# Kernel tuning notes

Measured on AMD Instinct MI355X. Metric: run time of the kernel, lower is better.

## Reference

```python
import jax, jax.numpy as jnp
import numpy as np

B, IN, H = 4096, 1024, 2048


def setup_inputs() -> dict:
    key = jax.random.key(0)
    k1, k2, k3, k4 = jax.random.split(key, 4)
    x = jax.random.normal(k1, (B, IN), dtype=jnp.float32)
    h_prev = jax.random.normal(k2, (B, H), dtype=jnp.float32)
    c_prev = jax.random.normal(k3, (B, H), dtype=jnp.float32)
    # Fused weight for the 5 gate Linears (Wf, Wi, Wc, Wo, We), columns stacked.
    # Scaled like PyTorch Linear default init (~uniform(-1/sqrt(fan_in))).
    W = jax.random.normal(k4, (IN + H, 5 * H), dtype=jnp.float32) / jnp.sqrt(jnp.float32(IN + H))
    b = jnp.zeros((5 * H,), dtype=jnp.float32)
    return {"x": x, "h_prev": h_prev, "c_prev": c_prev, "W": W, "b": b}


def reference(x, h_prev, c_prev, W, b):
    combined = jnp.concatenate([x, h_prev], axis=1)          # [B, IN+H]
    z = combined @ W + b                                      # [B, 5H] single fused GEMM
    f, i, c_hat, o, e = jnp.split(z, 5, axis=1)
    ft = jax.nn.sigmoid(f)
    it = jax.nn.sigmoid(i)
    ct_hat = jnp.tanh(c_hat)
    ot = jax.nn.sigmoid(o)
    et = jax.nn.sigmoid(e)
    ct = ft * c_prev + it * ct_hat
    ht = ot * jnp.tanh(ct)
    ht = et * jnp.exp(ht) + (1.0 - et) * ht
    return ht, ct
```

## Files before the change

### kernel.cpp

```cpp
#include <hip/hip_runtime.h>
#include <hip/hip_bf16.h>
#include <stdint.h>

#define B_  4096
#define IN_ 1024
#define H_  2048
#define K_  (IN_ + H_)
#define N_  (5 * H_)

#define BM 128
#define BJ 32
#define BK 32
#define NT 96

typedef __attribute__((ext_vector_type(8))) short   short8;
typedef __attribute__((ext_vector_type(4))) float   f32x4;
typedef __attribute__((ext_vector_type(8))) unsigned short ushort8;

__device__ __forceinline__ unsigned short f2bf(float f) {
  union { float f; unsigned u; } cv; cv.f = f;
  unsigned u = cv.u;
  u += 0x7fffu + ((u >> 16) & 1u);
  return (unsigned short)(u >> 16);
}

__device__ __forceinline__ void async16(const unsigned short* g, unsigned short* l) {
  __builtin_amdgcn_global_load_lds(
      (const __attribute__((address_space(1))) unsigned int*)g,
      (__attribute__((address_space(3))) unsigned int*)(void*)l,
      16, 0, 0);
}

__device__ __forceinline__ float fsig(float x) {
  return __builtin_amdgcn_rcpf(1.f + __expf(-x));
}
__device__ __forceinline__ float ftanh(float x) {
  return 1.f - 2.f * __builtin_amdgcn_rcpf(__expf(2.f * x) + 1.f);
}

__global__ void build_combined(const float* __restrict__ x,
                               const float* __restrict__ h,
                               unsigned short* __restrict__ out) {
  const int row = blockIdx.x;
  const float4* xr = (const float4*)(x + (size_t)row * IN_);
  const float4* hr = (const float4*)(h + (size_t)row * H_);
  uint2* orow = (uint2*)(out + (size_t)row * K_);
  for (int c = threadIdx.x; c < K_ / 4; c += 256) {
    float4 v = (c < IN_ / 4) ? xr[c] : hr[c - IN_ / 4];
    uint2 p;
    p.x = (unsigned)f2bf(v.x) | ((unsigned)f2bf(v.y) << 16);
    p.y = (unsigned)f2bf(v.z) | ((unsigned)f2bf(v.w) << 16);
    orow[c] = p;
  }
}

__global__ __launch_bounds__(256) void transpose_convert(
    const float* __restrict__ W, unsigned short* __restrict__ Wt) {
  __shared__ float tile[64][65];
  const int n0 = blockIdx.x * 64;
  const int k0 = blockIdx.y * 64;
  const int t  = threadIdx.x;

  const int r0 = t >> 4;
  const int c4 = t & 15;
  #pragma unroll
  for (int i = 0; i < 4; ++i) {
    const int kk = i * 16 + r0;
    const float4 v = *(const float4*)&W[(size_t)(k0 + kk) * N_ + n0 + c4 * 4];
    float* dst = &tile[kk][c4 * 4];
    dst[0] = v.x; dst[1] = v.y; dst[2] = v.z; dst[3] = v.w;
  }
  __syncthreads();

  #pragma unroll
  for (int i = 0; i < 2; ++i) {
    const int c2 = t + i * 256;
    const int nn = c2 >> 3;
    const int kc = (c2 & 7) * 8;
    ushort8 p;
    #pragma unroll
    for (int u = 0; u < 8; ++u) p[u] = f2bf(tile[kc + u][nn]);
    *(ushort8*)&Wt[(size_t)(n0 + nn) * K_ + k0 + kc] = p;
  }
}

__global__ __launch_bounds__(256, 3) void gemm_fused(
    const unsigned short* __restrict__ A,
    const unsigned short* __restrict__ Bt,
    const float* __restrict__ c_prev,
    const float* __restrict__ bias,
    float* __restrict__ out)
{
  __shared__ unsigned short As[2][BM * BK];
  __shared__ unsigned short Bs[2][5 * BJ * BK];

  const int tid  = threadIdx.x;
  const int wave = tid >> 6;
  const int lane = tid & 63;
  const int quad = lane >> 4;
  const int lr   = lane & 15;

  const int tile_m = blockIdx.x >> 6;
  const int tile_j = blockIdx.x & 63;
  const int m0 = tile_m * BM;
  const int j0 = tile_j * BJ;

  const int wm = (wave & 1) * 64;
  const int wn = (wave >> 1) * 16;

  f32x4 acc[4][5];
  #pragma unroll
  for (int mi = 0; mi < 4; ++mi)
    #pragma unroll
    for (int g = 0; g < 5; ++g)
      acc[mi][g] = (f32x4){0.f, 0.f, 0.f, 0.f};

  const int lrow4 = lane >> 2;
  const int scol  = ((lane & 3) ^ ((lane >> 3) & 3)) * 8;
  const size_t k16 = (size_t)16 * K_;

  const unsigned short* aP =
      A + ((size_t)(m0 + wave * 32 + lrow4)) * K_ + scol;
  const int aL0o = (wave * 32) * BK;
  const int aL1o = (wave * 32 + 16) * BK;

  const unsigned short* bBase = Bt + ((size_t)(j0 + lrow4)) * K_ + scol;
  const unsigned short* bP0 = bBase + (size_t)wave * H_ * K_;
  const unsigned short* bP2 = bBase + ((size_t)4 * H_ + wave * 16) * K_;
  const int bL0o = (wave * 32) * BK;
  const int bL1o = (wave * 32 + 16) * BK;
  const int bL2o = ((8 + wave) * 16) * BK;
  const bool doTail = (wave < 2);

  #define STAGE(tt, bb) do {                          \
    const int ko_ = (tt) * BK;                        \
    async16(aP + ko_,        &As[(bb)][aL0o]);        \
    async16(aP + k16 + ko_,  &As[(bb)][aL1o]);        \
    async16(bP0 + ko_,       &Bs[(bb)][bL0o]);        \
    async16(bP0 + k16 + ko_, &Bs[(bb)][bL1o]);        \
    if (doTail) async16(bP2 + ko_, &Bs[(bb)][bL2o]);  \
  } while (0)

  STAGE(0, 0);
  STAGE(1, 1);

  const int rslot = (quad ^ ((lr >> 1) & 3)) * 8;

  #pragma unroll 2
  for (int t = 0; t < NT; ++t) {
    const int cur = t & 1;

    if (t == NT - 1)     asm volatile("s_waitcnt vmcnt(0)" ::: "memory");
    else if (doTail)     asm volatile("s_waitcnt vmcnt(5)" ::: "memory");
    else                 asm volatile("s_waitcnt vmcnt(4)" ::: "memory");
    __builtin_amdgcn_s_barrier();

    short8 af[4], bf[5];
    #pragma unroll
    for (int mi = 0; mi < 4; ++mi)
      af[mi] = *(const short8*)&As[cur][(wm + mi * 16 + lr) * BK + rslot];
    #pragma unroll
    for (int g = 0; g < 5; ++g)
      bf[g] = *(const short8*)&Bs[cur][(g * 32 + wn + lr) * BK + rslot];

    asm volatile("s_waitcnt lgkmcnt(0)" ::: "memory");
    __builtin_amdgcn_sched_barrier(0);
    __builtin_amdgcn_s_barrier();

    if (t < NT - 2) STAGE(t + 2, cur);
    __builtin_amdgcn_sched_barrier(0);

    __builtin_amdgcn_s_setprio(1);
    #pragma unroll
    for (int mi = 0; mi < 4; ++mi)
      #pragma unroll
      for (int g = 0; g < 5; ++g)
        acc[mi][g] = __builtin_amdgcn_mfma_f32_16x16x32_bf16(
            af[mi], bf[g], acc[mi][g], 0, 0, 0);
    __builtin_amdgcn_s_setprio(0);
  }
  #undef STAGE

  const int col = j0 + wn + lr;
  float bb[5];
  #pragma unroll
  for (int g = 0; g < 5; ++g) bb[g] = bias[g * H_ + col];

  #pragma unroll
  for (int mi = 0; mi < 4; ++mi) {
    const int rbase = m0 + wm + mi * 16 + quad * 4;
    float cp[4];
    #pragma unroll
    for (int r = 0; r < 4; ++r)
      cp[r] = c_prev[(size_t)(rbase + r) * H_ + col];
    #pragma unroll
    for (int r = 0; r < 4; ++r) {
      const float ft = fsig(acc[mi][0][r] + bb[0]);
      const float it = fsig(acc[mi][1][r] + bb[1]);
      const float ch = ftanh(acc[mi][2][r] + bb[2]);
      const float ot = fsig(acc[mi][3][r] + bb[3]);
      const float et = fsig(acc[mi][4][r] + bb[4]);
      const float ct = ft * cp[r] + it * ch;
      const float th = ftanh(ct);
      float ht = ot * th;
      ht = et * __expf(ht) + (1.f - et) * ht;
      out[(size_t)(rbase + r) * H_ + col] = ht;
      out[(size_t)B_ * H_ + (size_t)(rbase + r) * H_ + col] = ct;
    }
  }
}

extern "C" void kernel_launch(void* const* d_in, const int* in_sizes, int n_in,
                              void* d_out, int out_size, void* d_ws, size_t ws_size,
                              hipStream_t stream) {
  const float* x = (const float*)d_in[0];
  const float* h = (const float*)d_in[1];
  const float* c = (const float*)d_in[2];
  const float* W = (const float*)d_in[3];
  const float* b = (const float*)d_in[4];
  float* out = (float*)d_out;

  char* ws = (char*)d_ws;
  unsigned short* combined = (unsigned short*)ws;
  unsigned short* Wt = (unsigned short*)(ws + (size_t)25165824);

  build_combined<<<B_, 256, 0, stream>>>(x, h, combined);
  transpose_convert<<<dim3(N_ / 64, K_ / 64), 256, 0, stream>>>(W, Wt);
  gemm_fused<<<(B_ / BM) * (H_ / BJ), 256, 0, stream>>>(combined, Wt, c, b, out);
}
```

Baseline: 526.2 us.

## Enlarge GEMM tile to 256x160 with 8 waves and BK=64 split-phase pipeline

The fused GEMM now uses 512-thread blocks covering 256 rows and BK=64 per stage instead of 128 rows and BK=32. Each K step is split into two half-steps, with A and B loads for the next stage interleaved between them, and the LDS swizzle is changed to an 8-way XOR. The larger tile raises reuse of B across more rows and halves the number of loop iterations and barriers. In exchange it uses more LDS per block and more barriers inside each step, and the grid shrinks to 1024 blocks, which may lower occupancy or cause tail imbalance.

New measurement: 539.1 us. +2.5%, slower.

```diff
diff --git a/kernel.cpp b/kernel.cpp
--- a/kernel.cpp
+++ b/kernel.cpp
@@ -8,10 +8,10 @@
 #define K_  (IN_ + H_)
 #define N_  (5 * H_)
 
-#define BM 128
-#define BJ 32
-#define BK 32
-#define NT 96
+#define BM2 256
+#define BJ2 32
+#define BK2 64
+#define NT2 48
 
 typedef __attribute__((ext_vector_type(8))) short   short8;
 typedef __attribute__((ext_vector_type(4))) float   f32x4;
@@ -84,15 +84,15 @@
   }
 }
 
-__global__ __launch_bounds__(256, 3) void gemm_fused(
+__global__ __launch_bounds__(512, 2) void gemm_fused(
     const unsigned short* __restrict__ A,
     const unsigned short* __restrict__ Bt,
     const float* __restrict__ c_prev,
     const float* __restrict__ bias,
     float* __restrict__ out)
 {
-  __shared__ unsigned short As[2][BM * BK];
-  __shared__ unsigned short Bs[2][5 * BJ * BK];
+  __shared__ unsigned short As[2][BM2 * BK2];
+  __shared__ unsigned short Bs[2][5 * BJ2 * BK2];
 
   const int tid  = threadIdx.x;
   const int wave = tid >> 6;
@@ -102,11 +102,11 @@
 
   const int tile_m = blockIdx.x >> 6;
   const int tile_j = blockIdx.x & 63;
-  const int m0 = tile_m * BM;
-  const int j0 = tile_j * BJ;
-
-  const int wm = (wave & 1) * 64;
-  const int wn = (wave >> 1) * 16;
+  const int m0 = tile_m * BM2;
+  const int j0 = tile_j * BJ2;
+
+  const int wm = (wave & 3) * 64;
+  const int wn = (wave >> 2) * 16;
 
   f32x4 acc[4][5];
   #pragma unroll
@@ -115,59 +115,64 @@
     for (int g = 0; g < 5; ++g)
       acc[mi][g] = (f32x4){0.f, 0.f, 0.f, 0.f};
 
-  const int lrow4 = lane >> 2;
-  const int scol  = ((lane & 3) ^ ((lane >> 3) & 3)) * 8;
-  const size_t k16 = (size_t)16 * K_;
-
-  const unsigned short* aP =
-      A + ((size_t)(m0 + wave * 32 + lrow4)) * K_ + scol;
-  const int aL0o = (wave * 32) * BK;
-  const int aL1o = (wave * 32 + 16) * BK;
-
-  const unsigned short* bBase = Bt + ((size_t)(j0 + lrow4)) * K_ + scol;
-  const unsigned short* bP0 = bBase + (size_t)wave * H_ * K_;
-  const unsigned short* bP2 = bBase + ((size_t)4 * H_ + wave * 16) * K_;
-  const int bL0o = (wave * 32) * BK;
-  const int bL1o = (wave * 32 + 16) * BK;
-  const int bL2o = ((8 + wave) * 16) * BK;
-  const bool doTail = (wave < 2);
-
-  #define STAGE(tt, bb) do {                          \
-    const int ko_ = (tt) * BK;                        \
-    async16(aP + ko_,        &As[(bb)][aL0o]);        \
-    async16(aP + k16 + ko_,  &As[(bb)][aL1o]);        \
-    async16(bP0 + ko_,       &Bs[(bb)][bL0o]);        \
-    async16(bP0 + k16 + ko_, &Bs[(bb)][bL1o]);        \
-    if (doTail) async16(bP2 + ko_, &Bs[(bb)][bL2o]);  \
+  const int lrow8 = lane >> 3;
+  const int sw8   = ((lane & 7) ^ lrow8) * 8;
+
+  const unsigned short* aSrc =
+      A + (size_t)(m0 + 8 * wave + lrow8) * K_ + sw8;
+
+  const bool doTail = (wave < 4);
+  const int cB0 = wave;
+  const int cB1 = wave + 8;
+  const int cB2 = doTail ? wave + 16 : wave;
+  const unsigned short* bSrc0 =
+      Bt + (size_t)((cB0 >> 2) * H_ + j0 + (cB0 & 3) * 8 + lrow8) * K_ + sw8;
+  const unsigned short* bSrc1 =
+      Bt + (size_t)((cB1 >> 2) * H_ + j0 + (cB1 & 3) * 8 + lrow8) * K_ + sw8;
+  const unsigned short* bSrc2 =
+      Bt + (size_t)((cB2 >> 2) * H_ + j0 + (cB2 & 3) * 8 + lrow8) * K_ + sw8;
+
+  #define STAGE_A(ko_, bb) do {                                        \
+    async16(aSrc + (ko_),                    &As[bb][512 * wave]);     \
+    async16(aSrc + (size_t) 64 * K_ + (ko_), &As[bb][512 * (wave + 8)]);  \
+    async16(aSrc + (size_t)128 * K_ + (ko_), &As[bb][512 * (wave + 16)]); \
+    async16(aSrc + (size_t)192 * K_ + (ko_), &As[bb][512 * (wave + 24)]); \
   } while (0)
-
-  STAGE(0, 0);
-  STAGE(1, 1);
-
-  const int rslot = (quad ^ ((lr >> 1) & 3)) * 8;
+  #define STAGE_B(ko_, bb) do {                                        \
+    async16(bSrc0 + (ko_), &Bs[bb][512 * cB0]);                        \
+    async16(bSrc1 + (ko_), &Bs[bb][512 * cB1]);                        \
+    if (doTail) async16(bSrc2 + (ko_), &Bs[bb][512 * cB2]);            \
+  } while (0)
+
+  STAGE_A((size_t)0, 0);
+  STAGE_B((size_t)0, 0);
+
+  const int rs0 = ((0 + quad) ^ (lr & 7)) * 8;
+  const int rs1 = ((4 + quad) ^ (lr & 7)) * 8;
+  const int aR[4] = { (wm + 0 * 16 + lr) * BK2, (wm + 1 * 16 + lr) * BK2,
+                      (wm + 2 * 16 + lr) * BK2, (wm + 3 * 16 + lr) * BK2 };
+  const int bR[5] = { (0 * 32 + wn + lr) * BK2, (1 * 32 + wn + lr) * BK2,
+                      (2 * 32 + wn + lr) * BK2, (3 * 32 + wn + lr) * BK2,
+                      (4 * 32 + wn + lr) * BK2 };
 
   #pragma unroll 2
-  for (int t = 0; t < NT; ++t) {
+  for (int t = 0; t < NT2; ++t) {
     const int cur = t & 1;
-
-    if (t == NT - 1)     asm volatile("s_waitcnt vmcnt(0)" ::: "memory");
-    else if (doTail)     asm volatile("s_waitcnt vmcnt(5)" ::: "memory");
-    else                 asm volatile("s_waitcnt vmcnt(4)" ::: "memory");
-    __builtin_amdgcn_s_barrier();
-
-    short8 af[4], bf[5];
-    #pragma unroll
-    for (int mi = 0; mi < 4; ++mi)
-      af[mi] = *(const short8*)&As[cur][(wm + mi * 16 + lr) * BK + rslot];
+    const size_t koN = (size_t)(t + 1) * BK2;
+
+    if (t < NT2 - 1) STAGE_A(koN, cur ^ 1);
+    if (t == NT2 - 1) asm volatile("s_waitcnt vmcnt(0)" ::: "memory");
+    else              asm volatile("s_waitcnt vmcnt(4)" ::: "memory");
+    __builtin_amdgcn_s_barrier();
+
+    short8 af0[4], bf0[5];
+    #pragma unroll
+    for (int mi = 0; mi < 4; ++mi)
+      af0[mi] = *(const short8*)&As[cur][aR[mi] + rs0];
     #pragma unroll
     for (int g = 0; g < 5; ++g)
-      bf[g] = *(const short8*)&Bs[cur][(g * 32 + wn + lr) * BK + rslot];
-
+      bf0[g] = *(const short8*)&Bs[cur][bR[g] + rs0];
     asm volatile("s_waitcnt lgkmcnt(0)" ::: "memory");
-    __builtin_amdgcn_sched_barrier(0);
-    __builtin_amdgcn_s_barrier();
-
-    if (t < NT - 2) STAGE(t + 2, cur);
     __builtin_amdgcn_sched_barrier(0);
 
     __builtin_amdgcn_s_setprio(1);
@@ -176,10 +181,34 @@
       #pragma unroll
       for (int g = 0; g < 5; ++g)
         acc[mi][g] = __builtin_amdgcn_mfma_f32_16x16x32_bf16(
-            af[mi], bf[g], acc[mi][g], 0, 0, 0);
+            af0[mi], bf0[g], acc[mi][g], 0, 0, 0);
     __builtin_amdgcn_s_setprio(0);
-  }
-  #undef STAGE
+    __builtin_amdgcn_s_barrier();
+
+    if (t < NT2 - 1) STAGE_B(koN, cur ^ 1);
+    short8 af1[4], bf1[5];
+    #pragma unroll
+    for (int mi = 0; mi < 4; ++mi)
+      af1[mi] = *(const short8*)&As[cur][aR[mi] + rs1];
+    #pragma unroll
+    for (int g = 0; g < 5; ++g)
+      bf1[g] = *(const short8*)&Bs[cur][bR[g] + rs1];
+    __builtin_amdgcn_s_barrier();
+    asm volatile("s_waitcnt lgkmcnt(0)" ::: "memory");
+    __builtin_amdgcn_sched_barrier(0);
+
+    __builtin_amdgcn_s_setprio(1);
+    #pragma unroll
+    for (int mi = 0; mi < 4; ++mi)
+      #pragma unroll
+      for (int g = 0; g < 5; ++g)
+        acc[mi][g] = __builtin_amdgcn_mfma_f32_16x16x32_bf16(
+            af1[mi], bf1[g], acc[mi][g], 0, 0, 0);
+    __builtin_amdgcn_s_setprio(0);
+    __builtin_amdgcn_s_barrier();
+  }
+  #undef STAGE_A
+  #undef STAGE_B
 
   const int col = j0 + wn + lr;
   float bb[5];
@@ -226,5 +255,5 @@
 
   build_combined<<<B_, 256, 0, stream>>>(x, h, combined);
   transpose_convert<<<dim3(N_ / 64, K_ / 64), 256, 0, stream>>>(W, Wt);
-  gemm_fused<<<(B_ / BM) * (H_ / BJ), 256, 0, stream>>>(combined, Wt, c, b, out);
-}
+  gemm_fused<<<(B_ / BM2) * (H_ / BJ2), 512, 0, stream>>>(combined, Wt, c, b, out);
+}
```
